# Optimization experiments

Hardware: AMD Instinct MI355X
Metric: run time of the kernel (lower is better)

Reference implementation:

```python
import jax, jax.numpy as jnp
import numpy as np

DIM = 256
NUM_HEADS = 4
HEAD_DIM = DIM // NUM_HEADS
EPS = 1e-5


def setup_inputs() -> dict:
    key = jax.random.key(0)
    ks = jax.random.split(key, 8)
    B, N, C = 8, 2048, DIM
    s = 0.02
    return {
        "x": jax.random.normal(ks[0], (B, N, C), jnp.float32),
        "qkv_w": jax.random.normal(ks[1], (C, 3 * C), jnp.float32) * s,
        "qkv_b": jnp.zeros((3 * C,), jnp.float32),
        "proj_w": jax.random.normal(ks[2], (C, C), jnp.float32) * s,
        "proj_b": jnp.zeros((C,), jnp.float32),
        "ln1_g": jnp.ones((C,), jnp.float32),
        "ln1_b": jnp.zeros((C,), jnp.float32),
        "ln2_g": jnp.ones((C,), jnp.float32),
        "ln2_b": jnp.zeros((C,), jnp.float32),
        "mlp_w1": jax.random.normal(ks[3], (C, 2 * C), jnp.float32) * s,
        "mlp_b1": jnp.zeros((2 * C,), jnp.float32),
        "mlp_w2": jax.random.normal(ks[4], (2 * C, C), jnp.float32) * s,
        "mlp_b2": jnp.zeros((C,), jnp.float32),
    }


def _layernorm(x, g, b):
    mu = jnp.mean(x, axis=-1, keepdims=True)
    var = jnp.mean(jnp.square(x - mu), axis=-1, keepdims=True)
    return (x - mu) * jax.lax.rsqrt(var + EPS) * g + b


def reference(x, qkv_w, qkv_b, proj_w, proj_b, ln1_g, ln1_b, ln2_g, ln2_b,
              mlp_w1, mlp_b1, mlp_w2, mlp_b2):
    B, N, C = x.shape
    H, D = NUM_HEADS, HEAD_DIM
    shortcut = x
    h = _layernorm(x, ln1_g, ln1_b)
    qkv = (h @ qkv_w + qkv_b).reshape(B, N, 3, H, D)
    q = qkv[:, :, 0].transpose(0, 2, 1, 3)  # [B,H,N,D]
    k = qkv[:, :, 1].transpose(0, 2, 1, 3)
    v = qkv[:, :, 2].transpose(0, 2, 1, 3)
    attn = jnp.einsum('bhnd,bhmd->bhnm', q, k) * (D ** -0.5)
    attn = jax.nn.softmax(attn, axis=-1)  # dropout = identity (eval mode)
    o = jnp.einsum('bhnm,bhmd->bhnd', attn, v)
    o = o.transpose(0, 2, 1, 3).reshape(B, N, C)
    x = o @ proj_w + proj_b + shortcut
    h2 = _layernorm(x, ln2_g, ln2_b)
    mlp = jax.nn.gelu(h2 @ mlp_w1 + mlp_b1, approximate=False) @ mlp_w2 + mlp_b2
    return x + mlp
```

## Files before the change

kernel.cpp:

```cpp
#include <hip/hip_runtime.h>

typedef __bf16 bf16;
typedef __bf16 bf16x8 __attribute__((ext_vector_type(8)));
typedef __bf16 bf16x4 __attribute__((ext_vector_type(4)));
typedef float  f32x4  __attribute__((ext_vector_type(4)));
typedef unsigned u32x2 __attribute__((ext_vector_type(2)));

typedef __attribute__((address_space(1))) const void GASV;
typedef __attribute__((address_space(3))) void LASV;

__device__ __forceinline__ void gload16(const void* g, void* l) {
  __builtin_amdgcn_global_load_lds((GASV*)g, (LASV*)l, 16, 0, 0);
}

constexpr float CEXP = 0.125f * 1.44269504088896340736f;

__global__ __launch_bounds__(256) void prep_fused(const float* __restrict__ qkv_w,
                                                  const float* __restrict__ proj_w,
                                                  const float* __restrict__ w1,
                                                  const float* __restrict__ w2,
                                                  bf16* __restrict__ Wtqkv,
                                                  bf16* __restrict__ WtP,
                                                  bf16* __restrict__ Wt1,
                                                  bf16* __restrict__ Wt2,
                                                  const float* __restrict__ x,
                                                  const float* __restrict__ gam,
                                                  const float* __restrict__ bet,
                                                  bf16* __restrict__ hout) {
  __shared__ float td[32][33];
  const int blk = blockIdx.x;
  const int tid = threadIdx.x;
  if (blk >= 512) {
    const int lane = tid & 63;
    const int w = tid >> 6;
    const size_t row = (size_t)(blk - 512) * 4 + w;
    const float4 v = *(const float4*)(x + row * 256 + lane * 4);
    float s1 = v.x + v.y + v.z + v.w;
    float s2 = v.x * v.x + v.y * v.y + v.z * v.z + v.w * v.w;
#pragma unroll
    for (int m = 1; m < 64; m <<= 1) {
      s1 += __shfl_xor(s1, m);
      s2 += __shfl_xor(s2, m);
    }
    const float mu = s1 * (1.0f / 256.0f);
    const float var = s2 * (1.0f / 256.0f) - mu * mu;
    const float rs = rsqrtf(var + 1e-5f);
    const float4 g4 = *(const float4*)(gam + lane * 4);
    const float4 b4 = *(const float4*)(bet + lane * 4);
    bf16x4 o;
    o[0] = (bf16)((v.x - mu) * rs * g4.x + b4.x);
    o[1] = (bf16)((v.y - mu) * rs * g4.y + b4.y);
    o[2] = (bf16)((v.z - mu) * rs * g4.z + b4.z);
    o[3] = (bf16)((v.w - mu) * rs * g4.w + b4.w);
    *(bf16x4*)(hout + row * 256 + lane * 4) = o;
    return;
  }
  const int t = blk;
  const float* src;
  bf16* dst;
  int Kin, Nin, kt, nt;
  if (t < 192)      { src = qkv_w; dst = Wtqkv; Kin = 256; Nin = 768; kt = t & 7;          nt = t >> 3; }
  else if (t < 256) { src = proj_w; dst = WtP;  Kin = 256; Nin = 256; kt = (t - 192) & 7;  nt = (t - 192) >> 3; }
  else if (t < 384) { src = w1;    dst = Wt1;   Kin = 256; Nin = 512; kt = (t - 256) & 7;  nt = (t - 256) >> 3; }
  else              { src = w2;    dst = Wt2;   Kin = 512; Nin = 256; kt = (t - 384) & 15; nt = (t - 384) >> 4; }
  {
    const int r = tid >> 3, c4 = (tid & 7) << 2;
    const float4 v = *(const float4*)(src + (size_t)(kt * 32 + r) * Nin + nt * 32 + c4);
    td[r][c4 + 0] = v.x; td[r][c4 + 1] = v.y; td[r][c4 + 2] = v.z; td[r][c4 + 3] = v.w;
  }
  __syncthreads();
  {
    const int n = tid >> 3, k4 = (tid & 7) << 2;
    bf16x4 o;
#pragma unroll
    for (int i = 0; i < 4; ++i) o[i] = (bf16)td[k4 + i][n];
    *(bf16x4*)(dst + (size_t)(nt * 32 + n) * Kin + kt * 32 + k4) = o;
  }
}

__global__ __launch_bounds__(256) void ln_fwd(const float* __restrict__ x,
                                              const float* __restrict__ gam,
                                              const float* __restrict__ bet,
                                              bf16* __restrict__ out) {
  const int lane = threadIdx.x & 63;
  const int w = threadIdx.x >> 6;
  const size_t row = (size_t)blockIdx.x * 4 + w;
  const float4 v = *(const float4*)(x + row * 256 + lane * 4);
  float s1 = v.x + v.y + v.z + v.w;
  float s2 = v.x * v.x + v.y * v.y + v.z * v.z + v.w * v.w;
#pragma unroll
  for (int m = 1; m < 64; m <<= 1) {
    s1 += __shfl_xor(s1, m);
    s2 += __shfl_xor(s2, m);
  }
  const float mu = s1 * (1.0f / 256.0f);
  const float var = s2 * (1.0f / 256.0f) - mu * mu;
  const float rs = rsqrtf(var + 1e-5f);
  const float4 g4 = *(const float4*)(gam + lane * 4);
  const float4 b4 = *(const float4*)(bet + lane * 4);
  bf16x4 o;
  o[0] = (bf16)((v.x - mu) * rs * g4.x + b4.x);
  o[1] = (bf16)((v.y - mu) * rs * g4.y + b4.y);
  o[2] = (bf16)((v.z - mu) * rs * g4.z + b4.z);
  o[3] = (bf16)((v.w - mu) * rs * g4.w + b4.w);
  *(bf16x4*)(out + row * 256 + lane * 4) = o;
}

template <int EPI, int NB>
__device__ __forceinline__ void gemm_core(bf16* __restrict__ ldsA, bf16* __restrict__ ldsB,
                                          const bf16* __restrict__ A,
                                          const bf16* __restrict__ Bt,
                                          const float* __restrict__ bias,
                                          const float* __restrict__ res,
                                          void* __restrict__ outp,
                                          int M, int N, int K, int bid) {
  const int tid = threadIdx.x;
  const int lane = tid & 63;
  const int W = tid >> 6;
  const int wm = W >> 2, wn = W & 3;
  const int qi = lane & 15, g = lane >> 4;
  const int nbm = M >> 7;
  const int bm = bid % nbm;
  const int bn = bid / nbm;
  const int m0 = bm << 7, n0 = bn << 7;
  const int nk = K >> 6;

  const char* asrc[2];
  const char* bsrc[2];
#pragma unroll
  for (int p = 0; p < 2; ++p) {
    const int s = p * 8 + W;
    const int row = (s >> 3) * 64 + ((s >> 1) & 3) * 16 + qi;
    const int kb = (s & 1) * 64 + g * 16;
    asrc[p] = (const char*)(A + (size_t)(m0 + row) * K) + kb;
    bsrc[p] = (const char*)(Bt + (size_t)(n0 + row) * K) + kb;
  }

  f32x4 acc[4][2];
#pragma unroll
  for (int i = 0; i < 4; ++i)
#pragma unroll
    for (int j = 0; j < 2; ++j) acc[i][j] = (f32x4){0.f, 0.f, 0.f, 0.f};

  auto stage = [&](int sl) {
#pragma unroll
    for (int p = 0; p < 2; ++p) {
      gload16(asrc[p], (char*)ldsA + sl * 16384 + (p * 8 + W) * 1024);
      gload16(bsrc[p], (char*)ldsB + sl * 16384 + (p * 8 + W) * 1024);
      asrc[p] += 128;
      bsrc[p] += 128;
    }
  };

  if constexpr (NB == 2) {
    stage(0);
    asm volatile("s_waitcnt vmcnt(0)" ::: "memory");
  } else {
    stage(0);
    stage(1);
    asm volatile("s_waitcnt vmcnt(4)" ::: "memory");
  }
  __builtin_amdgcn_s_barrier();

  int cur = 0, nxt = (NB == 2) ? 1 : 2;
  for (int t = 0; t < nk; ++t) {
    if constexpr (NB == 2) {
      if (t + 1 < nk) stage(nxt);
    }
    const char* pa = (const char*)ldsA + cur * 16384 + wm * 8192 + lane * 16;
    const char* pb = (const char*)ldsB + cur * 16384 + lane * 16;
    bf16x8 av[4][2], bv[2][2];
#pragma unroll
    for (int f = 0; f < 4; ++f)
#pragma unroll
      for (int ks = 0; ks < 2; ++ks)
        av[f][ks] = *(const bf16x8*)(pa + (f * 2 + ks) * 1024);
#pragma unroll
    for (int fn = 0; fn < 2; ++fn)
#pragma unroll
      for (int ks = 0; ks < 2; ++ks) {
        const int r16 = wn * 2 + fn;
        bv[fn][ks] = *(const bf16x8*)(pb + ((r16 >> 2) * 8 + (r16 & 3) * 2 + ks) * 1024);
      }
    if constexpr (NB == 3) {
      if (t + 2 < nk) stage(nxt);
    }
    __builtin_amdgcn_s_setprio(1);
#pragma unroll
    for (int fm = 0; fm < 4; ++fm)
#pragma unroll
      for (int fn = 0; fn < 2; ++fn) {
        acc[fm][fn] = __builtin_amdgcn_mfma_f32_16x16x32_bf16(av[fm][0], bv[fn][0], acc[fm][fn], 0, 0, 0);
        acc[fm][fn] = __builtin_amdgcn_mfma_f32_16x16x32_bf16(av[fm][1], bv[fn][1], acc[fm][fn], 0, 0, 0);
      }
    __builtin_amdgcn_s_setprio(0);
    if constexpr (NB == 2) {
      asm volatile("s_waitcnt vmcnt(0)" ::: "memory");
    } else {
      if (t + 2 < nk) {
        asm volatile("s_waitcnt vmcnt(4)" ::: "memory");
      } else {
        asm volatile("s_waitcnt vmcnt(0)" ::: "memory");
      }
    }
    __builtin_amdgcn_s_barrier();
    cur = (cur == NB - 1) ? 0 : cur + 1;
    nxt = (nxt == NB - 1) ? 0 : nxt + 1;
  }

#pragma unroll
  for (int fm = 0; fm < 4; ++fm)
#pragma unroll
    for (int fn = 0; fn < 2; ++fn) {
      const int r0 = m0 + wm * 64 + fm * 16 + g * 4;
      const int c = n0 + wn * 32 + fn * 16 + qi;
#pragma unroll
      for (int j = 0; j < 4; ++j) {
        const int r = r0 + j;
        const float v = acc[fm][fn][j];
        if constexpr (EPI == 0) {
          ((bf16*)outp)[(size_t)r * N + c] = (bf16)(v + bias[c]);
        } else if constexpr (EPI == 1) {
          ((bf16*)outp)[(size_t)r * 2048 + ((size_t)(c >> 11)) * 524288 + (c & 2047)] =
              (bf16)(v + bias[r]);
        } else if constexpr (EPI == 2) {
          ((float*)outp)[(size_t)r * N + c] = v + bias[c] + res[(size_t)r * N + c];
        } else {
          const float u = v + bias[c];
          ((bf16*)outp)[(size_t)r * N + c] = (bf16)(u * 0.5f * (1.0f + erff(u * 0.70710678118f)));
        }
      }
    }
}

__global__ __launch_bounds__(512) void gemm_qkv_fused(const bf16* __restrict__ h,
                                                      const bf16* __restrict__ Wtqkv,
                                                      const float* __restrict__ qkv_b,
                                                      bf16* __restrict__ qkb,
                                                      bf16* __restrict__ vT) {
  __shared__ bf16 ldsA[2 * 8192];
  __shared__ bf16 ldsB[2 * 8192];
  const int bid = (int)blockIdx.x;
  if (bid < 512) {
    gemm_core<0, 2>(ldsA, ldsB, h, Wtqkv, qkv_b, nullptr, qkb, 16384, 512, 256, bid);
  } else {
    gemm_core<1, 2>(ldsA, ldsB, Wtqkv + 512 * 256, h, qkv_b + 512, nullptr, vT,
                    256, 16384, 256, bid - 512);
  }
}

template <int EPI, int NB>
__global__ __launch_bounds__(512) void gemm_one(const bf16* __restrict__ A,
                                                const bf16* __restrict__ Bt,
                                                const float* __restrict__ bias,
                                                const float* __restrict__ res,
                                                void* __restrict__ outp,
                                                int M, int N, int K) {
  __shared__ bf16 ldsA[NB * 8192];
  __shared__ bf16 ldsB[NB * 8192];
  gemm_core<EPI, NB>(ldsA, ldsB, A, Bt, bias, res, outp, M, N, K, (int)blockIdx.x);
}

__global__ __launch_bounds__(256) void attn_fwd(const bf16* __restrict__ qk,
                                                const bf16* __restrict__ vT,
                                                bf16* __restrict__ po0,
                                                bf16* __restrict__ po1,
                                                float* __restrict__ pstats) {
  __shared__ bf16 Kl[2][4096];
  __shared__ bf16 Vl[2][4096];
  __shared__ bf16 Pl[4][1024];
  const int tid = threadIdx.x;
  const int lane = tid & 63;
  const int w = tid >> 6;
  const int g = lane >> 4;
  const int qi = lane & 15;
  const int bid = (int)blockIdx.x;
  const int bh = bid & 31;
  const int qt = (bid >> 5) & 15;
  const int s = bid >> 9;
  const int b = bh >> 2, h = bh & 3;

  const size_t qrow0 = (size_t)b * 2048 + qt * 128 + w * 32 + qi;
  bf16x8 qf[2][2];
#pragma unroll
  for (int f = 0; f < 2; ++f) {
    const bf16* qp = qk + (qrow0 + f * 16) * 512 + h * 64 + g * 8;
    qf[f][0] = *(const bf16x8*)qp;
    qf[f][1] = *(const bf16x8*)(qp + 32);
  }

  float mrun[2] = {0.f, 0.f};
  float lsum[2] = {0.f, 0.f};
  f32x4 o[4][2];
#pragma unroll
  for (int i = 0; i < 4; ++i)
#pragma unroll
    for (int f = 0; f < 2; ++f) o[i][f] = (f32x4){0.f, 0.f, 0.f, 0.f};

  constexpr float THR = 8.0f / CEXP;

  const char* kbase = (const char*)qk + ((size_t)b * 2048) * 1024 + 512 + h * 128 +
                      (size_t)s * 16 * 65536;
  const char* vbase = (const char*)vT + (size_t)bh * 262144 + (size_t)s * 16 * 128;
  const char* ks[2];
  const char* vs[2];
#pragma unroll
  for (int i = 0; i < 2; ++i) {
    const int fk = i * 2 + (w >> 1);
    const int half = w & 1;
    ks[i] = kbase + (fk * 16 + qi) * 1024 + half * 64 + g * 16;
    vs[i] = vbase + (size_t)(fk * 16 + qi) * 4096 + half * 64 + g * 16;
  }
  char* const pw = (char*)&Pl[w][0];
  int paddrb[2];
#pragma unroll
  for (int bb = 0; bb < 2; ++bb)
    paddrb[bb] = (bb * 2 + (g >> 1)) * 256 + qi * 16 + (g & 1) * 8;
  const char* const prd = pw + lane * 16;

  auto stage = [&](int slot) {
    char* kd = (char*)&Kl[0][0] + slot * 8192 + w * 1024;
    char* vd = (char*)&Vl[0][0] + slot * 8192 + w * 1024;
    gload16(ks[0], kd);
    gload16(ks[1], kd + 4096);
    gload16(vs[0], vd);
    gload16(vs[1], vd + 4096);
    ks[0] += 65536; ks[1] += 65536;
    vs[0] += 128;   vs[1] += 128;
  };

  stage(0);
  asm volatile("s_waitcnt vmcnt(0)" ::: "memory");
  __builtin_amdgcn_s_barrier();

  for (int t = 0; t < 16; ++t) {
    if (t < 15) stage((t + 1) & 1);
    const char* kb = (const char*)&Kl[0][0] + (t & 1) * 8192 + lane * 16;
    f32x4 st[4][2];
    __builtin_amdgcn_s_setprio(1);
#pragma unroll
    for (int fk = 0; fk < 4; ++fk) {
      const bf16x8 k0 = *(const bf16x8*)(kb + fk * 2048);
      const bf16x8 k1 = *(const bf16x8*)(kb + fk * 2048 + 1024);
#pragma unroll
      for (int f = 0; f < 2; ++f) {
        f32x4 z = (f32x4){0.f, 0.f, 0.f, 0.f};
        st[fk][f] = __builtin_amdgcn_mfma_f32_16x16x32_bf16(k0, qf[f][0], z, 0, 0, 0);
        st[fk][f] = __builtin_amdgcn_mfma_f32_16x16x32_bf16(k1, qf[f][1], st[fk][f], 0, 0, 0);
      }
    }
    __builtin_amdgcn_s_setprio(0);
    float pmax[2];
#pragma unroll
    for (int f = 0; f < 2; ++f) {
      float m0 = fmaxf(fmaxf(st[0][f][0], st[0][f][1]), fmaxf(st[0][f][2], st[0][f][3]));
      float m1 = fmaxf(fmaxf(st[1][f][0], st[1][f][1]), fmaxf(st[1][f][2], st[1][f][3]));
      float m2 = fmaxf(fmaxf(st[2][f][0], st[2][f][1]), fmaxf(st[2][f][2], st[2][f][3]));
      float m3 = fmaxf(fmaxf(st[3][f][0], st[3][f][1]), fmaxf(st[3][f][2], st[3][f][3]));
      pmax[f] = fmaxf(fmaxf(m0, m1), fmaxf(m2, m3));
    }
    if (!__all(pmax[0] <= mrun[0] + THR && pmax[1] <= mrun[1] + THR)) {
#pragma unroll
      for (int f = 0; f < 2; ++f) {
        float mt = fmaxf(pmax[f], __shfl_xor(pmax[f], 16));
        mt = fmaxf(mt, __shfl_xor(mt, 32));
        const float mnew = fmaxf(mrun[f], mt);
        const float alpha = exp2f(CEXP * (mrun[f] - mnew));
        lsum[f] *= alpha;
#pragma unroll
        for (int fd = 0; fd < 4; ++fd)
#pragma unroll
          for (int j = 0; j < 4; ++j) o[fd][f][j] *= alpha;
        mrun[f] = mnew;
      }
    }
    unsigned pk[4][2][2];
#pragma unroll
    for (int f = 0; f < 2; ++f) {
      const float negcm = -CEXP * mrun[f];
      float ts = 0.f;
#pragma unroll
      for (int fk = 0; fk < 4; ++fk)
#pragma unroll
        for (int jp = 0; jp < 2; ++jp) {
          const float p0 = exp2f(fmaf(st[fk][f][2 * jp], CEXP, negcm));
          const float p1 = exp2f(fmaf(st[fk][f][2 * jp + 1], CEXP, negcm));
          ts += p0 + p1;
          union { bf16 h2[2]; unsigned u; } cv;
          cv.h2[0] = (bf16)p0;
          cv.h2[1] = (bf16)p1;
          pk[fk][f][jp] = cv.u;
        }
      lsum[f] += ts;
    }
    const char* vb = (const char*)&Vl[0][0] + (t & 1) * 8192 + lane * 16;
#pragma unroll
    for (int ksl = 0; ksl < 2; ++ksl) {
#pragma unroll
      for (int bb = 0; bb < 2; ++bb) {
        const int fk = 2 * ksl + bb;
#pragma unroll
        for (int f = 0; f < 2; ++f) {
          u32x2 pv2;
          pv2[0] = pk[fk][f][0];
          pv2[1] = pk[fk][f][1];
          *(u32x2*)(pw + f * 1024 + paddrb[bb]) = pv2;
        }
      }
      bf16x8 pa[2];
#pragma unroll
      for (int f = 0; f < 2; ++f) pa[f] = *(const bf16x8*)(prd + f * 1024);
      __builtin_amdgcn_s_setprio(1);
#pragma unroll
      for (int fd = 0; fd < 4; ++fd) {
        const bf16x8 vv = *(const bf16x8*)(vb + fd * 2048 + ksl * 1024);
#pragma unroll
        for (int f = 0; f < 2; ++f)
          o[fd][f] = __builtin_amdgcn_mfma_f32_16x16x32_bf16(vv, pa[f], o[fd][f], 0, 0, 0);
      }
      __builtin_amdgcn_s_setprio(0);
    }
    asm volatile("s_waitcnt vmcnt(0)" ::: "memory");
    __builtin_amdgcn_s_barrier();
  }

#pragma unroll
  for (int f = 0; f < 2; ++f) {
    float l = lsum[f];
    l += __shfl_xor(l, 16);
    l += __shfl_xor(l, 32);
    lsum[f] = l;
  }
  if (g == 0) {
#pragma unroll
    for (int f = 0; f < 2; ++f) {
      float2 sv;
      sv.x = mrun[f];
      sv.y = lsum[f];
      *(float2*)(pstats + (((size_t)s * 32 + bh) * 2048 + qt * 128 + w * 32 + f * 16 + qi) * 2) = sv;
    }
  }
  bf16* const pob = s ? po1 : po0;
#pragma unroll
  for (int f = 0; f < 2; ++f) {
    bf16* const orow = pob + (qrow0 + f * 16) * 256 + h * 64 + g * 4;
#pragma unroll
    for (int fd = 0; fd < 4; ++fd) {
      bf16x4 ov;
#pragma unroll
      for (int j = 0; j < 4; ++j) ov[j] = (bf16)o[fd][f][j];
      *(bf16x4*)(orow + fd * 16) = ov;
    }
  }
}

__global__ __launch_bounds__(256) void attn_merge(const bf16* __restrict__ po0,
                                                  const bf16* __restrict__ po1,
                                                  const float* __restrict__ pstats,
                                                  bf16* __restrict__ ob) {
  const int idx = blockIdx.x * 256 + threadIdx.x;
  const int r = idx >> 6;
  const int cq = (idx & 63) * 4;
  const int h = cq >> 6;
  const int bh = (r >> 11) * 4 + h;
  const int ql = r & 2047;
  const float2 s0 = *(const float2*)(pstats + (((size_t)bh) * 2048 + ql) * 2);
  const float2 s1 = *(const float2*)(pstats + (((size_t)32 + bh) * 2048 + ql) * 2);
  const float M = fmaxf(s0.x, s1.x);
  const float a0 = exp2f(CEXP * (s0.x - M));
  const float a1 = exp2f(CEXP * (s1.x - M));
  const float inv = 1.0f / (s0.y * a0 + s1.y * a1);
  const bf16x4 p0 = *(const bf16x4*)(po0 + (size_t)r * 256 + cq);
  const bf16x4 p1 = *(const bf16x4*)(po1 + (size_t)r * 256 + cq);
  bf16x4 ov;
#pragma unroll
  for (int j = 0; j < 4; ++j)
    ov[j] = (bf16)(((float)p0[j] * a0 + (float)p1[j] * a1) * inv);
  *(bf16x4*)(ob + (size_t)r * 256 + cq) = ov;
}

extern "C" void kernel_launch(void* const* d_in, const int* in_sizes, int n_in,
                              void* d_out, int out_size, void* d_ws, size_t ws_size,
                              hipStream_t stream) {
  const float* x      = (const float*)d_in[0];
  const float* qkv_w  = (const float*)d_in[1];
  const float* qkv_b  = (const float*)d_in[2];
  const float* proj_w = (const float*)d_in[3];
  const float* proj_b = (const float*)d_in[4];
  const float* ln1_g  = (const float*)d_in[5];
  const float* ln1_b  = (const float*)d_in[6];
  const float* ln2_g  = (const float*)d_in[7];
  const float* ln2_b  = (const float*)d_in[8];
  const float* mlp_w1 = (const float*)d_in[9];
  const float* mlp_b1 = (const float*)d_in[10];
  const float* mlp_w2 = (const float*)d_in[11];
  const float* mlp_b2 = (const float*)d_in[12];
  float* out = (float*)d_out;

  char* ws = (char*)d_ws;
  bf16* Wtqkv = (bf16*)(ws);
  bf16* WtP   = (bf16*)(ws + 393216);
  bf16* Wt1   = (bf16*)(ws + 524288);
  bf16* Wt2   = (bf16*)(ws + 786432);
  bf16* h     = (bf16*)(ws + 1048576);
  bf16* qkb   = (bf16*)(ws + 9437184);
  bf16* vT    = (bf16*)(ws + 26214400);
  bf16* po1   = (bf16*)(ws + 34603008);
  float* x2   = (float*)(ws + 42991616);
  float* pstats = (float*)(ws + 59768832);
  bf16* po0  = h;
  bf16* obuf = vT;
  bf16* a1 = qkb;
  bf16* h2 = h;

  prep_fused<<<4608, 256, 0, stream>>>(qkv_w, proj_w, mlp_w1, mlp_w2, Wtqkv, WtP, Wt1, Wt2,
                                       x, ln1_g, ln1_b, h);
  gemm_qkv_fused<<<768, 512, 0, stream>>>(h, Wtqkv, qkv_b, qkb, vT);
  attn_fwd<<<1024, 256, 0, stream>>>(qkb, vT, po0, po1, pstats);
  attn_merge<<<4096, 256, 0, stream>>>(po0, po1, pstats, obuf);
  gemm_one<2, 3><<<256, 512, 0, stream>>>(obuf, WtP, proj_b, x, x2, 16384, 256, 256);
  ln_fwd<<<4096, 256, 0, stream>>>(x2, ln2_g, ln2_b, h2);
  gemm_one<3, 2><<<512, 512, 0, stream>>>(h2, Wt1, mlp_b1, nullptr, a1, 16384, 512, 256);
  gemm_one<2, 3><<<256, 512, 0, stream>>>(a1, Wt2, mlp_b2, x2, out, 16384, 256, 512);
}
```

Baseline: 161.2 us.

## Fuse split-KV attention merge into projection GEMM A-tile loading

Removes the separate attn_merge kernel and its intermediate buffer by having a new projection GEMM read both partial attention outputs and softmax stats, combine them in registers, and write the merged bf16 A tile into LDS. This saves one launch plus a full write and read of the merged activation. In exchange, the GEMM's A path uses register loads and ALU work instead of direct global-to-LDS copies. It also reads po0 and po1 twice, once per N-block, and uses a new 2-stage pipeline rather than the generic gemm_core.

```diff
diff --git a/kernel.cpp b/kernel.cpp
--- a/kernel.cpp
+++ b/kernel.cpp
@@ -261,6 +261,128 @@
   gemm_core<EPI, NB>(ldsA, ldsB, A, Bt, bias, res, outp, M, N, K, (int)blockIdx.x);
 }
 
+__global__ __launch_bounds__(512) void gemm_proj_merge(const bf16* __restrict__ po0,
+                                                       const bf16* __restrict__ po1,
+                                                       const float* __restrict__ pstats,
+                                                       const bf16* __restrict__ Bt,
+                                                       const float* __restrict__ bias,
+                                                       const float* __restrict__ res,
+                                                       float* __restrict__ outp) {
+  __shared__ bf16 Al[2][8192];
+  __shared__ bf16 Bl[2][8192];
+  const int tid = threadIdx.x;
+  const int lane = tid & 63;
+  const int W = tid >> 6;
+  const int wm = W >> 2, wn = W & 3;
+  const int qi = lane & 15, g = lane >> 4;
+  const int bm = (int)blockIdx.x & 127;
+  const int bn = (int)blockIdx.x >> 7;
+  const int m0 = bm << 7, n0 = bn << 7;
+
+  int rowg[2];
+  const char* asrc[2];
+  const char* bsrc[2];
+#pragma unroll
+  for (int p = 0; p < 2; ++p) {
+    const int s = p * 8 + W;
+    const int row = (s >> 3) * 64 + ((s >> 1) & 3) * 16 + qi;
+    const int kb = (s & 1) * 64 + g * 16;
+    rowg[p] = m0 + row;
+    asrc[p] = (const char*)po0 + (size_t)(m0 + row) * 512 + kb;
+    bsrc[p] = (const char*)(Bt + (size_t)(n0 + row) * 256) + kb;
+  }
+  const size_t dpo = (size_t)((const char*)po1 - (const char*)po0);
+
+  f32x4 acc[4][2];
+#pragma unroll
+  for (int i = 0; i < 4; ++i)
+#pragma unroll
+    for (int j = 0; j < 2; ++j) acc[i][j] = (f32x4){0.f, 0.f, 0.f, 0.f};
+
+  bf16x8 pa0v[2], pa1v[2];
+  float2 sst0[2], sst1[2];
+
+  auto MAload = [&](int t) {
+#pragma unroll
+    for (int p = 0; p < 2; ++p) {
+      gload16(bsrc[p], (char*)&Bl[t & 1][0] + (p * 8 + W) * 1024);
+      bsrc[p] += 128;
+      pa0v[p] = *(const bf16x8*)(asrc[p]);
+      pa1v[p] = *(const bf16x8*)(asrc[p] + dpo);
+      asrc[p] += 128;
+      const int bh = ((rowg[p] >> 11) << 2) + t;
+      const int ql = rowg[p] & 2047;
+      sst0[p] = *(const float2*)(pstats + ((size_t)bh * 2048 + ql) * 2);
+      sst1[p] = *(const float2*)(pstats + ((size_t)(bh + 32) * 2048 + ql) * 2);
+    }
+  };
+  auto MAwrite = [&](int t) {
+#pragma unroll
+    for (int p = 0; p < 2; ++p) {
+      const float mx = fmaxf(sst0[p].x, sst1[p].x);
+      float a0 = exp2f(CEXP * (sst0[p].x - mx));
+      float a1 = exp2f(CEXP * (sst1[p].x - mx));
+      const float inv = 1.0f / (sst0[p].y * a0 + sst1[p].y * a1);
+      a0 *= inv;
+      a1 *= inv;
+      bf16x8 wv;
+#pragma unroll
+      for (int j = 0; j < 8; ++j)
+        wv[j] = (bf16)((float)pa0v[p][j] * a0 + (float)pa1v[p][j] * a1);
+      *(bf16x8*)((char*)&Al[t & 1][0] + (p * 8 + W) * 1024 + lane * 16) = wv;
+    }
+  };
+
+  MAload(0);
+  MAwrite(0);
+  asm volatile("s_waitcnt vmcnt(0) lgkmcnt(0)" ::: "memory");
+  __builtin_amdgcn_s_barrier();
+
+  for (int t = 0; t < 4; ++t) {
+    if (t + 1 < 4) MAload(t + 1);
+    const char* pa = (const char*)&Al[t & 1][0] + wm * 8192 + lane * 16;
+    const char* pb = (const char*)&Bl[t & 1][0] + lane * 16;
+    bf16x8 av[4][2], bv[2][2];
+#pragma unroll
+    for (int f = 0; f < 4; ++f)
+#pragma unroll
+      for (int ks = 0; ks < 2; ++ks)
+        av[f][ks] = *(const bf16x8*)(pa + (f * 2 + ks) * 1024);
+#pragma unroll
+    for (int fn = 0; fn < 2; ++fn)
+#pragma unroll
+      for (int ks = 0; ks < 2; ++ks) {
+        const int r16 = wn * 2 + fn;
+        bv[fn][ks] = *(const bf16x8*)(pb + ((r16 >> 2) * 8 + (r16 & 3) * 2 + ks) * 1024);
+      }
+    __builtin_amdgcn_s_setprio(1);
+#pragma unroll
+    for (int fm = 0; fm < 4; ++fm)
+#pragma unroll
+      for (int fn = 0; fn < 2; ++fn) {
+        acc[fm][fn] = __builtin_amdgcn_mfma_f32_16x16x32_bf16(av[fm][0], bv[fn][0], acc[fm][fn], 0, 0, 0);
+        acc[fm][fn] = __builtin_amdgcn_mfma_f32_16x16x32_bf16(av[fm][1], bv[fn][1], acc[fm][fn], 0, 0, 0);
+      }
+    __builtin_amdgcn_s_setprio(0);
+    if (t + 1 < 4) MAwrite(t + 1);
+    asm volatile("s_waitcnt vmcnt(0) lgkmcnt(0)" ::: "memory");
+    __builtin_amdgcn_s_barrier();
+  }
+
+#pragma unroll
+  for (int fm = 0; fm < 4; ++fm)
+#pragma unroll
+    for (int fn = 0; fn < 2; ++fn) {
+      const int r0 = m0 + wm * 64 + fm * 16 + g * 4;
+      const int c = n0 + wn * 32 + fn * 16 + qi;
+#pragma unroll
+      for (int j = 0; j < 4; ++j) {
+        const int r = r0 + j;
+        outp[(size_t)r * 256 + c] = acc[fm][fn][j] + bias[c] + res[(size_t)r * 256 + c];
+      }
+    }
+}
+
 __global__ __launch_bounds__(256) void attn_fwd(const bf16* __restrict__ qk,
                                                 const bf16* __restrict__ vT,
                                                 bf16* __restrict__ po0,
@@ -454,31 +576,6 @@
   }
 }
 
-__global__ __launch_bounds__(256) void attn_merge(const bf16* __restrict__ po0,
-                                                  const bf16* __restrict__ po1,
-                                                  const float* __restrict__ pstats,
-                                                  bf16* __restrict__ ob) {
-  const int idx = blockIdx.x * 256 + threadIdx.x;
-  const int r = idx >> 6;
-  const int cq = (idx & 63) * 4;
-  const int h = cq >> 6;
-  const int bh = (r >> 11) * 4 + h;
-  const int ql = r & 2047;
-  const float2 s0 = *(const float2*)(pstats + (((size_t)bh) * 2048 + ql) * 2);
-  const float2 s1 = *(const float2*)(pstats + (((size_t)32 + bh) * 2048 + ql) * 2);
-  const float M = fmaxf(s0.x, s1.x);
-  const float a0 = exp2f(CEXP * (s0.x - M));
-  const float a1 = exp2f(CEXP * (s1.x - M));
-  const float inv = 1.0f / (s0.y * a0 + s1.y * a1);
-  const bf16x4 p0 = *(const bf16x4*)(po0 + (size_t)r * 256 + cq);
-  const bf16x4 p1 = *(const bf16x4*)(po1 + (size_t)r * 256 + cq);
-  bf16x4 ov;
-#pragma unroll
-  for (int j = 0; j < 4; ++j)
-    ov[j] = (bf16)(((float)p0[j] * a0 + (float)p1[j] * a1) * inv);
-  *(bf16x4*)(ob + (size_t)r * 256 + cq) = ov;
-}
-
 extern "C" void kernel_launch(void* const* d_in, const int* in_sizes, int n_in,
                               void* d_out, int out_size, void* d_ws, size_t ws_size,
                               hipStream_t stream) {
@@ -508,8 +605,7 @@
   bf16* po1   = (bf16*)(ws + 34603008);
   float* x2   = (float*)(ws + 42991616);
   float* pstats = (float*)(ws + 59768832);
-  bf16* po0  = h;
-  bf16* obuf = vT;
+  bf16* po0 = h;
   bf16* a1 = qkb;
   bf16* h2 = h;
 
@@ -517,8 +613,7 @@
                                        x, ln1_g, ln1_b, h);
   gemm_qkv_fused<<<768, 512, 0, stream>>>(h, Wtqkv, qkv_b, qkb, vT);
   attn_fwd<<<1024, 256, 0, stream>>>(qkb, vT, po0, po1, pstats);
-  attn_merge<<<4096, 256, 0, stream>>>(po0, po1, pstats, obuf);
-  gemm_one<2, 3><<<256, 512, 0, stream>>>(obuf, WtP, proj_b, x, x2, 16384, 256, 256);
+  gemm_proj_merge<<<256, 512, 0, stream>>>(po0, po1, pstats, WtP, proj_b, x, x2);
   ln_fwd<<<4096, 256, 0, stream>>>(x2, ln2_g, ln2_b, h2);
   gemm_one<3, 2><<<512, 512, 0, stream>>>(h2, Wt1, mlp_b1, nullptr, a1, 16384, 512, 256);
   gemm_one<2, 3><<<256, 512, 0, stream>>>(a1, Wt2, mlp_b2, x2, out, 16384, 256, 512);
```

Measured after the change: 160.5 us. About the same (-0.5%).

## Fuse split-KV attention merge into attn_fwd via intra-block LDS reduction

Applied to the files above, without the earlier changes.

The two KV-split halves of each query tile now run as two 4-wave groups inside a single 512-thread block instead of as separate blocks. Each group keeps its own K/V double-buffer slab, and the stats and partial outputs are exchanged through LDS so the rescale-and-merge happens in-kernel. This removes the separate attn_merge launch and the global round-trip of the bf16 partial outputs and stats. In exchange the grid drops to 512 larger blocks with more LDS per block, which may reduce occupancy and latency hiding.

```diff
diff --git a/kernel.cpp b/kernel.cpp
--- a/kernel.cpp
+++ b/kernel.cpp
@@ -261,26 +261,25 @@
   gemm_core<EPI, NB>(ldsA, ldsB, A, Bt, bias, res, outp, M, N, K, (int)blockIdx.x);
 }
 
-__global__ __launch_bounds__(256) void attn_fwd(const bf16* __restrict__ qk,
+__global__ __launch_bounds__(512) void attn_fwd(const bf16* __restrict__ qk,
                                                 const bf16* __restrict__ vT,
-                                                bf16* __restrict__ po0,
-                                                bf16* __restrict__ po1,
-                                                float* __restrict__ pstats) {
-  __shared__ bf16 Kl[2][4096];
-  __shared__ bf16 Vl[2][4096];
-  __shared__ bf16 Pl[4][1024];
+                                                bf16* __restrict__ ob) {
+  __shared__ bf16 Kl[2][2][4096];
+  __shared__ bf16 Vl[2][2][4096];
+  __shared__ bf16 Pl[8][1024];
   const int tid = threadIdx.x;
   const int lane = tid & 63;
   const int w = tid >> 6;
+  const int grp = w >> 2;
+  const int wq = w & 3;
   const int g = lane >> 4;
   const int qi = lane & 15;
   const int bid = (int)blockIdx.x;
   const int bh = bid & 31;
-  const int qt = (bid >> 5) & 15;
-  const int s = bid >> 9;
+  const int qt = bid >> 5;
   const int b = bh >> 2, h = bh & 3;
 
-  const size_t qrow0 = (size_t)b * 2048 + qt * 128 + w * 32 + qi;
+  const size_t qrow0 = (size_t)b * 2048 + qt * 128 + wq * 32 + qi;
   bf16x8 qf[2][2];
 #pragma unroll
   for (int f = 0; f < 2; ++f) {
@@ -300,17 +299,19 @@
   constexpr float THR = 8.0f / CEXP;
 
   const char* kbase = (const char*)qk + ((size_t)b * 2048) * 1024 + 512 + h * 128 +
-                      (size_t)s * 16 * 65536;
-  const char* vbase = (const char*)vT + (size_t)bh * 262144 + (size_t)s * 16 * 128;
+                      (size_t)grp * 65536;
+  const char* vbase = (const char*)vT + (size_t)bh * 262144 + (size_t)grp * 128;
   const char* ks[2];
   const char* vs[2];
 #pragma unroll
   for (int i = 0; i < 2; ++i) {
-    const int fk = i * 2 + (w >> 1);
-    const int half = w & 1;
+    const int fk = i * 2 + (wq >> 1);
+    const int half = wq & 1;
     ks[i] = kbase + (fk * 16 + qi) * 1024 + half * 64 + g * 16;
     vs[i] = vbase + (size_t)(fk * 16 + qi) * 4096 + half * 64 + g * 16;
   }
+  char* const kslab = (char*)&Kl[grp][0][0];
+  char* const vslab = (char*)&Vl[grp][0][0];
   char* const pw = (char*)&Pl[w][0];
   int paddrb[2];
 #pragma unroll
@@ -319,14 +320,14 @@
   const char* const prd = pw + lane * 16;
 
   auto stage = [&](int slot) {
-    char* kd = (char*)&Kl[0][0] + slot * 8192 + w * 1024;
-    char* vd = (char*)&Vl[0][0] + slot * 8192 + w * 1024;
+    char* kd = kslab + slot * 8192 + wq * 1024;
+    char* vd = vslab + slot * 8192 + wq * 1024;
     gload16(ks[0], kd);
     gload16(ks[1], kd + 4096);
     gload16(vs[0], vd);
     gload16(vs[1], vd + 4096);
-    ks[0] += 65536; ks[1] += 65536;
-    vs[0] += 128;   vs[1] += 128;
+    ks[0] += 131072; ks[1] += 131072;
+    vs[0] += 256;    vs[1] += 256;
   };
 
   stage(0);
@@ -335,7 +336,7 @@
 
   for (int t = 0; t < 16; ++t) {
     if (t < 15) stage((t + 1) & 1);
-    const char* kb = (const char*)&Kl[0][0] + (t & 1) * 8192 + lane * 16;
+    const char* kb = kslab + (t & 1) * 8192 + lane * 16;
     f32x4 st[4][2];
     __builtin_amdgcn_s_setprio(1);
 #pragma unroll
@@ -393,7 +394,7 @@
         }
       lsum[f] += ts;
     }
-    const char* vb = (const char*)&Vl[0][0] + (t & 1) * 8192 + lane * 16;
+    const char* vb = vslab + (t & 1) * 8192 + lane * 16;
 #pragma unroll
     for (int ksl = 0; ksl < 2; ++ksl) {
 #pragma unroll
@@ -431,52 +432,40 @@
     l += __shfl_xor(l, 32);
     lsum[f] = l;
   }
-  if (g == 0) {
-#pragma unroll
-    for (int f = 0; f < 2; ++f) {
-      float2 sv;
-      sv.x = mrun[f];
-      sv.y = lsum[f];
-      *(float2*)(pstats + (((size_t)s * 32 + bh) * 2048 + qt * 128 + w * 32 + f * 16 + qi) * 2) = sv;
-    }
-  }
-  bf16* const pob = s ? po1 : po0;
+  f32x4 stv;
+  stv[0] = mrun[0]; stv[1] = lsum[0]; stv[2] = mrun[1]; stv[3] = lsum[1];
+  *(f32x4*)((char*)&Pl[0][0] + w * 1024 + lane * 16) = stv;
+  char* const oslab = (char*)&Kl[0][0][0] + w * 4096;
+#pragma unroll
+  for (int fd2 = 0; fd2 < 2; ++fd2) {
+    const int wf = grp ? fd2 : 2 + fd2;
+#pragma unroll
+    for (int f = 0; f < 2; ++f)
+      *(f32x4*)(oslab + (fd2 * 2 + f) * 1024 + lane * 16) = o[wf][f];
+  }
+  __syncthreads();
+  const int p = w ^ 4;
+  const f32x4 pst = *(const f32x4*)((char*)&Pl[0][0] + p * 1024 + lane * 16);
+  const char* const pslab = (char*)&Kl[0][0][0] + p * 4096;
 #pragma unroll
   for (int f = 0; f < 2; ++f) {
-    bf16* const orow = pob + (qrow0 + f * 16) * 256 + h * 64 + g * 4;
-#pragma unroll
-    for (int fd = 0; fd < 4; ++fd) {
+    const float mme = mrun[f], lme = lsum[f];
+    const float mot = pst[2 * f], lot = pst[2 * f + 1];
+    const float ms = fmaxf(mme, mot);
+    const float am = exp2f(CEXP * (mme - ms));
+    const float ao = exp2f(CEXP * (mot - ms));
+    const float inv = 1.0f / (lme * am + lot * ao);
+#pragma unroll
+    for (int fd2 = 0; fd2 < 2; ++fd2) {
+      const int kf = grp ? 2 + fd2 : fd2;
+      const f32x4 po = *(const f32x4*)(pslab + (fd2 * 2 + f) * 1024 + lane * 16);
       bf16x4 ov;
 #pragma unroll
-      for (int j = 0; j < 4; ++j) ov[j] = (bf16)o[fd][f][j];
-      *(bf16x4*)(orow + fd * 16) = ov;
-    }
-  }
-}
-
-__global__ __launch_bounds__(256) void attn_merge(const bf16* __restrict__ po0,
-                                                  const bf16* __restrict__ po1,
-                                                  const float* __restrict__ pstats,
-                                                  bf16* __restrict__ ob) {
-  const int idx = blockIdx.x * 256 + threadIdx.x;
-  const int r = idx >> 6;
-  const int cq = (idx & 63) * 4;
-  const int h = cq >> 6;
-  const int bh = (r >> 11) * 4 + h;
-  const int ql = r & 2047;
-  const float2 s0 = *(const float2*)(pstats + (((size_t)bh) * 2048 + ql) * 2);
-  const float2 s1 = *(const float2*)(pstats + (((size_t)32 + bh) * 2048 + ql) * 2);
-  const float M = fmaxf(s0.x, s1.x);
-  const float a0 = exp2f(CEXP * (s0.x - M));
-  const float a1 = exp2f(CEXP * (s1.x - M));
-  const float inv = 1.0f / (s0.y * a0 + s1.y * a1);
-  const bf16x4 p0 = *(const bf16x4*)(po0 + (size_t)r * 256 + cq);
-  const bf16x4 p1 = *(const bf16x4*)(po1 + (size_t)r * 256 + cq);
-  bf16x4 ov;
-#pragma unroll
-  for (int j = 0; j < 4; ++j)
-    ov[j] = (bf16)(((float)p0[j] * a0 + (float)p1[j] * a1) * inv);
-  *(bf16x4*)(ob + (size_t)r * 256 + cq) = ov;
+      for (int j = 0; j < 4; ++j)
+        ov[j] = (bf16)((o[kf][f][j] * am + po[j] * ao) * inv);
+      *(bf16x4*)(ob + (qrow0 + f * 16) * 256 + h * 64 + kf * 16 + g * 4) = ov;
+    }
+  }
 }
 
 extern "C" void kernel_launch(void* const* d_in, const int* in_sizes, int n_in,
@@ -505,19 +494,15 @@
   bf16* h     = (bf16*)(ws + 1048576);
   bf16* qkb   = (bf16*)(ws + 9437184);
   bf16* vT    = (bf16*)(ws + 26214400);
-  bf16* po1   = (bf16*)(ws + 34603008);
+  bf16* obuf  = (bf16*)(ws + 34603008);
   float* x2   = (float*)(ws + 42991616);
-  float* pstats = (float*)(ws + 59768832);
-  bf16* po0  = h;
-  bf16* obuf = vT;
   bf16* a1 = qkb;
   bf16* h2 = h;
 
   prep_fused<<<4608, 256, 0, stream>>>(qkv_w, proj_w, mlp_w1, mlp_w2, Wtqkv, WtP, Wt1, Wt2,
                                        x, ln1_g, ln1_b, h);
   gemm_qkv_fused<<<768, 512, 0, stream>>>(h, Wtqkv, qkv_b, qkb, vT);
-  attn_fwd<<<1024, 256, 0, stream>>>(qkb, vT, po0, po1, pstats);
-  attn_merge<<<4096, 256, 0, stream>>>(po0, po1, pstats, obuf);
+  attn_fwd<<<512, 512, 0, stream>>>(qkb, vT, obuf);
   gemm_one<2, 3><<<256, 512, 0, stream>>>(obuf, WtP, proj_b, x, x2, 16384, 256, 256);
   ln_fwd<<<4096, 256, 0, stream>>>(x2, ln2_g, ln2_b, h2);
   gemm_one<3, 2><<<512, 512, 0, stream>>>(h2, Wt1, mlp_b1, nullptr, a1, 16384, 512, 256);
```

New measurement: 170.3 us. 1.06x slower.
